# Optimization experiments

Hardware: AMD Instinct MI355X
Metric: run time of the kernel (lower is better)

The kernel has to match this reference:

```python
import jax, jax.numpy as jnp
import numpy as np

HID = 128
N_LAYERS = 6


def _init_linear(key, fan_in, fan_out, scale=None):
    kw, kb = jax.random.split(key)
    s = scale if scale is not None else (1.0 / np.sqrt(fan_in))
    W = jax.random.uniform(kw, (fan_in, fan_out), jnp.float32, -s, s)
    b = jnp.zeros((fan_out,), jnp.float32)
    return W, b


def setup_inputs() -> dict:
    key = jax.random.key(0)
    ks = jax.random.split(key, 16)
    N, E, EC = 50000, 600000, 100000
    x = jax.random.normal(ks[0], (N, 9), jnp.float32)
    edge_index = jax.random.randint(ks[1], (2, E), 0, N, jnp.int64)
    edge_attr = jax.random.normal(ks[2], (E, 11), jnp.float32)
    connectivity = jax.random.randint(ks[3], (EC, 2), 0, N, jnp.int64)
    bc_disp = (jax.random.uniform(ks[4], (N, 1)) < 0.1).astype(jnp.float32)
    prop_I22 = jax.random.uniform(ks[5], (EC,), jnp.float32)

    enc_W1, enc_b1 = _init_linear(ks[6], 9, HID)
    enc_W2, enc_b2 = _init_linear(ks[7], HID, HID)
    # per-layer GN params stacked along axis 0
    msg_in = 2 * HID + 11
    mk = jax.random.split(ks[8], N_LAYERS)
    uk = jax.random.split(ks[9], N_LAYERS)
    mk2 = jax.random.split(ks[10], N_LAYERS)
    msg_W1 = jnp.stack([_init_linear(mk[i], msg_in, HID)[0] for i in range(N_LAYERS)])
    msg_b1 = jnp.zeros((N_LAYERS, HID), jnp.float32)
    msg_W2 = jnp.stack([_init_linear(mk2[i], HID, HID)[0] for i in range(N_LAYERS)])
    msg_b2 = jnp.zeros((N_LAYERS, HID), jnp.float32)
    upd_W = jnp.stack([_init_linear(uk[i], 2 * HID, HID)[0] for i in range(N_LAYERS)])
    upd_b = jnp.zeros((N_LAYERS, HID), jnp.float32)

    ef_W1, ef_b1 = _init_linear(ks[11], 1 + 2 * HID, 64)
    ef_W2, ef_b2 = _init_linear(ks[12], 64, 64)
    ef_W3, ef_b3 = _init_linear(ks[13], 64, 3, scale=0.1 * np.sqrt(6.0 / (64 + 3)))

    return dict(x=x, edge_index=edge_index, edge_attr=edge_attr,
                connectivity=connectivity, bc_disp=bc_disp, prop_I22=prop_I22,
                n_quad_pts=5,
                enc_W1=enc_W1, enc_b1=enc_b1, enc_W2=enc_W2, enc_b2=enc_b2,
                msg_W1=msg_W1, msg_b1=msg_b1, msg_W2=msg_W2, msg_b2=msg_b2,
                upd_W=upd_W, upd_b=upd_b,
                ef_W1=ef_W1, ef_b1=ef_b1, ef_W2=ef_W2, ef_b2=ef_b2,
                ef_W3=ef_W3, ef_b3=ef_b3)


def reference(x, edge_index, edge_attr, connectivity, bc_disp, prop_I22, n_quad_pts,
              enc_W1, enc_b1, enc_W2, enc_b2,
              msg_W1, msg_b1, msg_W2, msg_b2, upd_W, upd_b,
              ef_W1, ef_b1, ef_W2, ef_b2, ef_W3, ef_b3):
    N = x.shape[0]
    silu = jax.nn.silu
    # encoder MLP
    h = silu(x @ enc_W1 + enc_b1)
    h = silu(h @ enc_W2 + enc_b2)
    src, dst = edge_index[0], edge_index[1]
    for l in range(N_LAYERS):
        m_in = jnp.concatenate([h[src], h[dst], edge_attr], axis=-1)  # (E, 2H+11)
        m = silu(m_in @ msg_W1[l] + msg_b1[l]) @ msg_W2[l] + msg_b2[l]
        agg = jax.ops.segment_sum(m, dst, num_segments=N)  # scatter-add
        h = jnp.concatenate([h, agg], axis=-1) @ upd_W[l] + upd_b[l] + h  # residual update
        h = silu(h)
    # continuous edge field evaluation
    n1, n2 = connectivity[:, 0], connectivity[:, 1]
    EC = connectivity.shape[0]
    xi_1d = jnp.linspace(0.0, 1.0, n_quad_pts, dtype=jnp.float32)
    xi = jnp.broadcast_to(xi_1d[None, :, None], (EC, n_quad_pts, 1))
    h_i = jnp.broadcast_to(h[n1][:, None, :], (EC, n_quad_pts, HID))
    h_j = jnp.broadcast_to(h[n2][:, None, :], (EC, n_quad_pts, HID))
    inp = jnp.concatenate([xi, h_i, h_j], axis=-1)  # (EC, n_pts, 1+2H)
    f = silu(inp @ ef_W1 + ef_b1)
    f = silu(f @ ef_W2 + ef_b2)
    fields = f @ ef_W3 + ef_b3  # (EC, n_pts, 3)
    # hard BCs
    bc_mask = bc_disp[:, 0]
    bc_i, bc_j = bc_mask[n1], bc_mask[n2]
    xi_vals = xi[..., 0]
    mask_i = 1.0 - bc_i[:, None] * (1.0 - xi_vals)
    mask_j = 1.0 - bc_j[:, None] * xi_vals
    fields = fields * (mask_i * mask_j)[..., None]
    return h, xi, fields, prop_I22
```

## Files before the change

kernel.cpp:

```cpp
#include <hip/hip_runtime.h>
#include <hip/hip_bf16.h>

#define HID 128
#define EA_DIM 11
#define MSG_IN (2 * HID + EA_DIM)
#define TILE_E 128
#define KCAP 272
#define KB (KCAP * 2)
#define MSG_LDS 139264

typedef __attribute__((ext_vector_type(8))) short short8;
typedef __attribute__((ext_vector_type(16))) float f32x16;
typedef __attribute__((ext_vector_type(4))) float float4v;

__device__ __forceinline__ float siluf(float x) { return x / (1.f + __expf(-x)); }
__device__ __forceinline__ short f2bf(float f) {
    __hip_bfloat16 h = __float2bfloat16(f);
    return *reinterpret_cast<short*>(&h);
}
__device__ __forceinline__ int crow(int r, int khalf) { return (r & 3) + 8 * (r >> 2) + 4 * khalf; }

__global__ __launch_bounds__(128) void encoder_kernel(
    const float* __restrict__ x, const float* __restrict__ W1, const float* __restrict__ b1,
    const float* __restrict__ W2, const float* __restrict__ b2,
    float* __restrict__ h, short* __restrict__ hb)
{
    int i = blockIdx.x, j = threadIdx.x;
    __shared__ float xs[9];
    __shared__ float t1[HID];
    if (j < 9) xs[j] = x[(size_t)i * 9 + j];
    __syncthreads();
    float acc = b1[j];
    #pragma unroll
    for (int k = 0; k < 9; ++k) acc = fmaf(xs[k], W1[k * HID + j], acc);
    t1[j] = siluf(acc);
    __syncthreads();
    float acc2 = b2[j];
    #pragma unroll 8
    for (int k = 0; k < HID; ++k) acc2 = fmaf(t1[k], W2[k * HID + j], acc2);
    float v = siluf(acc2);
    h[(size_t)i * HID + j] = v;
    if (hb) hb[(size_t)i * HID + j] = f2bf(v);
}

__global__ void convert_w_kernel(
    const float* __restrict__ msgW1, const float* __restrict__ msgW2,
    const float* __restrict__ updW,
    const float* __restrict__ efW1, const float* __restrict__ efW2, const float* __restrict__ efW3,
    short* __restrict__ w1t, short* __restrict__ w2t, short* __restrict__ updwt,
    short* __restrict__ efw1t, short* __restrict__ efw2t, short* __restrict__ efw3t, int nl)
{
    int gid = blockIdx.x * blockDim.x + threadIdx.x;
    int n1 = nl * 128 * (KCAP / 8);
    int n2 = nl * 128 * (HID / 8);
    int n3 = nl * 128 * 32;
    int n4 = 64 * 32, n5 = 64 * 8, n6 = 32 * 8;
    short8 v;
    if (gid < n1) {
        int c = gid % (KCAP / 8);
        int rem = gid / (KCAP / 8);
        int n = rem % 128, lay = rem / 128;
        #pragma unroll
        for (int j = 0; j < 8; ++j) {
            int k = c * 8 + j;
            v[j] = (k < MSG_IN) ? f2bf(msgW1[(size_t)lay * MSG_IN * HID + (size_t)k * HID + n]) : (short)0;
        }
        *(short8*)(w1t + ((size_t)lay * 128 + n) * KCAP + c * 8) = v;
    } else if (gid < n1 + n2) {
        int g = gid - n1;
        int c = g % (HID / 8);
        int rem = g / (HID / 8);
        int n = rem % 128, lay = rem / 128;
        #pragma unroll
        for (int j = 0; j < 8; ++j)
            v[j] = f2bf(msgW2[(size_t)lay * HID * HID + (size_t)(c * 8 + j) * HID + n]);
        *(short8*)(w2t + ((size_t)lay * 128 + n) * HID + c * 8) = v;
    } else if (gid < n1 + n2 + n3) {
        int g = gid - n1 - n2;
        int c = g & 31;
        int rem = g >> 5;
        int n = rem & 127, lay = rem >> 7;
        #pragma unroll
        for (int j = 0; j < 8; ++j)
            v[j] = f2bf(updW[(size_t)lay * 256 * 128 + (size_t)(c * 8 + j) * 128 + n]);
        *(short8*)(updwt + ((size_t)lay * 128 + n) * 256 + c * 8) = v;
    } else if (gid < n1 + n2 + n3 + n4) {
        int g = gid - n1 - n2 - n3;
        int c = g & 31, n = g >> 5;
        #pragma unroll
        for (int j = 0; j < 8; ++j)
            v[j] = f2bf(efW1[(size_t)(c * 8 + j + 1) * 64 + n]);
        *(short8*)(efw1t + (size_t)n * 256 + c * 8) = v;
    } else if (gid < n1 + n2 + n3 + n4 + n5) {
        int g = gid - n1 - n2 - n3 - n4;
        int c = g & 7, n = g >> 3;
        #pragma unroll
        for (int j = 0; j < 8; ++j)
            v[j] = f2bf(efW2[(size_t)(c * 8 + j) * 64 + n]);
        *(short8*)(efw2t + (size_t)n * 64 + c * 8) = v;
    } else if (gid < n1 + n2 + n3 + n4 + n5 + n6) {
        int g = gid - n1 - n2 - n3 - n4 - n5;
        int c = g & 7, n = g >> 3;
        #pragma unroll
        for (int j = 0; j < 8; ++j)
            v[j] = (n < 3) ? f2bf(efW3[(size_t)(c * 8 + j) * 3 + n]) : (short)0;
        *(short8*)(efw3t + (size_t)n * 64 + c * 8) = v;
    }
}

__global__ void hist_kernel(const int* __restrict__ ei, int* __restrict__ cnt, int E)
{
    for (int e = blockIdx.x * blockDim.x + threadIdx.x; e < E; e += gridDim.x * blockDim.x)
        atomicAdd(&cnt[ei[(size_t)E + e]], 1);
}
__global__ __launch_bounds__(256) void scanA_kernel(const int* __restrict__ cnt, int* __restrict__ btot, int N)
{
    __shared__ int s[256];
    int i = blockIdx.x * 256 + threadIdx.x;
    s[threadIdx.x] = (i < N) ? cnt[i] : 0;
    __syncthreads();
    for (int o = 128; o > 0; o >>= 1) {
        if (threadIdx.x < o) s[threadIdx.x] += s[threadIdx.x + o];
        __syncthreads();
    }
    if (threadIdx.x == 0) btot[blockIdx.x] = s[0];
}
__global__ __launch_bounds__(1024) void scanB_kernel(int* __restrict__ btot, int nb)
{
    __shared__ int s[1024];
    int t = threadIdx.x;
    int v = (t < nb) ? btot[t] : 0;
    s[t] = v;
    __syncthreads();
    for (int o = 1; o < 1024; o <<= 1) {
        int tv = 0;
        if (t >= o) tv = s[t - o];
        __syncthreads();
        s[t] += tv;
        __syncthreads();
    }
    if (t < nb) btot[t] = s[t] - v;
}
__global__ __launch_bounds__(256) void scanC_kernel(const int* __restrict__ cnt, const int* __restrict__ btot,
                                                    int* __restrict__ cur, int N)
{
    __shared__ int s[256];
    int i = blockIdx.x * 256 + threadIdx.x;
    int t = threadIdx.x;
    int v = (i < N) ? cnt[i] : 0;
    s[t] = v;
    __syncthreads();
    for (int o = 1; o < 256; o <<= 1) {
        int tv = 0;
        if (t >= o) tv = s[t - o];
        __syncthreads();
        s[t] += tv;
        __syncthreads();
    }
    if (i < N) cur[i] = btot[blockIdx.x] + s[t] - v;
}
__global__ void scatter_kernel(const int* __restrict__ ei, int* __restrict__ cur,
                               int* __restrict__ eord, int E)
{
    for (int e = blockIdx.x * blockDim.x + threadIdx.x; e < E; e += gridDim.x * blockDim.x) {
        int d = ei[(size_t)E + e];
        int p = atomicAdd(&cur[d], 1);
        eord[p] = e;
    }
}
__global__ void reorder_kernel(const int* __restrict__ ei, const float* __restrict__ ea,
                               const int* __restrict__ eord,
                               int* __restrict__ srcs_s, int* __restrict__ dsts_s,
                               short* __restrict__ ea_s, int E)
{
    for (int p = blockIdx.x * blockDim.x + threadIdx.x; p < E; p += gridDim.x * blockDim.x) {
        int es = eord[p];
        srcs_s[p] = ei[es];
        dsts_s[p] = ei[(size_t)E + es];
        short tv[16];
        #pragma unroll
        for (int j = 0; j < 16; ++j) tv[j] = 0;
        #pragma unroll
        for (int j = 0; j < EA_DIM; ++j) tv[j] = f2bf(ea[(size_t)es * EA_DIM + j]);
        short8 v0, v1;
        #pragma unroll
        for (int j = 0; j < 8; ++j) { v0[j] = tv[j]; v1[j] = tv[8 + j]; }
        *(short8*)(ea_s + (size_t)p * 16) = v0;
        *(short8*)(ea_s + (size_t)p * 16 + 8) = v1;
    }
}

__global__ __launch_bounds__(512, 1) void msg_mfma_kernel(
    const float* __restrict__ h, const short* __restrict__ hb,
    const int* __restrict__ ei, const float* __restrict__ ea,
    const int* __restrict__ srcs_s, const int* __restrict__ dsts_s, const short* __restrict__ ea_s,
    const short* __restrict__ w1t, const float* __restrict__ b1,
    const short* __restrict__ w2t, const float* __restrict__ b2,
    float* __restrict__ agg, int E, int ntiles)
{
    extern __shared__ char smem[];
    char* sA = smem + 69632;
    __shared__ int dsts[TILE_E];

    int tid = threadIdx.x, ln = tid & 63, wave = tid >> 6;
    int mh = wave & 1, nq4 = wave >> 1;
    int l31 = ln & 31, khalf = ln >> 5;

    {
        int row = tid & 127, grp = tid >> 7;
        for (int c = grp; c < 34; c += 4) {
            short8 v = *(const short8*)(w1t + (size_t)row * KCAP + c * 8);
            *(short8*)(smem + ((row * KB + c * 16) ^ ((row & 7) << 4))) = v;
        }
    }

    int col = nq4 * 32 + l31;
    float b1v = b1[col], b2v = b2[col];
    short8 zer;
    #pragma unroll
    for (int j = 0; j < 8; ++j) zer[j] = 0;
    int ar0 = mh * 64 + l31;
    const short8* w2r = (const short8*)(w2t + (size_t)col * HID);

    #pragma unroll 1
    for (int tile = blockIdx.x; tile < ntiles; tile += gridDim.x) {
        __syncthreads();

        {
            int r = tid >> 2, q = tid & 3;
            long ep = (long)tile * TILE_E + r;
            bool valid = ep < E;
            int idx = 0;
            if (valid) {
                if (ea_s) idx = (q < 2) ? srcs_s[ep] : dsts_s[ep];
                else      idx = (q < 2) ? ei[ep] : ei[(size_t)E + ep];
            }
            int half = q & 1;
            int dbase = (q >> 1) * 256 + half * 128;
            if (hb) {
                const short8* hr8 = (const short8*)(hb + (size_t)idx * HID + half * 64);
                #pragma unroll
                for (int c = 0; c < 8; ++c) {
                    short8 v = valid ? hr8[c] : zer;
                    *(short8*)(sA + ((r * KB + dbase + c * 16) ^ ((r & 7) << 4))) = v;
                }
            } else {
                const float* hr = h + (size_t)idx * HID + half * 64;
                #pragma unroll
                for (int c = 0; c < 8; ++c) {
                    short8 v = zer;
                    if (valid) {
                        float4v f0 = *(const float4v*)(hr + c * 8);
                        float4v f1 = *(const float4v*)(hr + c * 8 + 4);
                        #pragma unroll
                        for (int j = 0; j < 4; ++j) { v[j] = f2bf(f0[j]); v[4 + j] = f2bf(f1[j]); }
                    }
                    *(short8*)(sA + ((r * KB + dbase + c * 16) ^ ((r & 7) << 4))) = v;
                }
            }
            if (q == 2) dsts[r] = valid ? idx : -1;
            if (q == 3) {
                short8 v0 = zer, v1 = zer;
                if (valid) {
                    if (ea_s) {
                        v0 = *(const short8*)(ea_s + (size_t)ep * 16);
                        v1 = *(const short8*)(ea_s + (size_t)ep * 16 + 8);
                    } else {
                        short tv[16];
                        #pragma unroll
                        for (int j = 0; j < 16; ++j) tv[j] = 0;
                        #pragma unroll
                        for (int j = 0; j < EA_DIM; ++j) tv[j] = f2bf(ea[(size_t)ep * EA_DIM + j]);
                        #pragma unroll
                        for (int j = 0; j < 8; ++j) { v0[j] = tv[j]; v1[j] = tv[8 + j]; }
                    }
                }
                *(short8*)(sA + ((r * KB + 512) ^ ((r & 7) << 4))) = v0;
                *(short8*)(sA + ((r * KB + 528) ^ ((r & 7) << 4))) = v1;
            }
        }
        __syncthreads();

        f32x16 acc1[2] = {};
        for (int kk = 0; kk < 17; ++kk) {
            int kb = kk * 32 + khalf * 16;
            short8 a0 = *(short8*)(sA + ((ar0 * KB + kb) ^ ((ar0 & 7) << 4)));
            short8 a1 = *(short8*)(sA + (((ar0 + 32) * KB + kb) ^ (((ar0 + 32) & 7) << 4)));
            short8 w  = *(short8*)(smem + ((col * KB + kb) ^ ((col & 7) << 4)));
            acc1[0] = __builtin_amdgcn_mfma_f32_32x32x16_bf16(a0, w, acc1[0], 0, 0, 0);
            acc1[1] = __builtin_amdgcn_mfma_f32_32x32x16_bf16(a1, w, acc1[1], 0, 0, 0);
        }
        __syncthreads();

        #pragma unroll
        for (int mi = 0; mi < 2; ++mi)
            #pragma unroll
            for (int r = 0; r < 16; ++r) {
                float s = siluf(acc1[mi][r] + b1v);
                int row = mh * 64 + mi * 32 + crow(r, khalf);
                *(short*)(sA + ((row * 256 + col * 2) ^ ((row & 7) << 4))) = f2bf(s);
            }
        __syncthreads();

        f32x16 acc2[2];
        #pragma unroll
        for (int mi = 0; mi < 2; ++mi)
            #pragma unroll
            for (int r = 0; r < 16; ++r) acc2[mi][r] = b2v;
        for (int kk = 0; kk < 8; ++kk) {
            int kb = kk * 32 + khalf * 16;
            short8 a0 = *(short8*)(sA + ((ar0 * 256 + kb) ^ ((ar0 & 7) << 4)));
            short8 a1 = *(short8*)(sA + (((ar0 + 32) * 256 + kb) ^ (((ar0 + 32) & 7) << 4)));
            short8 w  = w2r[kk * 2 + khalf];
            acc2[0] = __builtin_amdgcn_mfma_f32_32x32x16_bf16(a0, w, acc2[0], 0, 0, 0);
            acc2[1] = __builtin_amdgcn_mfma_f32_32x32x16_bf16(a1, w, acc2[1], 0, 0, 0);
        }

        if (ea_s) {
            __syncthreads();
            #pragma unroll
            for (int mi = 0; mi < 2; ++mi)
                #pragma unroll
                for (int r = 0; r < 16; ++r) {
                    int row = mh * 64 + mi * 32 + crow(r, khalf);
                    *(float*)(sA + row * 512 + col * 4) = acc2[mi][r];
                }
            __syncthreads();
            {
                int c2 = tid & 63, g = tid >> 6;
                float s0 = 0.f, s1 = 0.f;
                int dprev = -1;
                #pragma unroll 1
                for (int rr = 0; rr < 16; ++rr) {
                    int row = g * 16 + rr;
                    int d = dsts[row];
                    float2 v = *(float2*)(sA + row * 512 + c2 * 8);
                    if (d != dprev) {
                        if (dprev >= 0) {
                            atomicAdd(agg + (size_t)dprev * HID + c2 * 2,     s0);
                            atomicAdd(agg + (size_t)dprev * HID + c2 * 2 + 1, s1);
                        }
                        s0 = 0.f; s1 = 0.f; dprev = d;
                    }
                    if (d >= 0) { s0 += v.x; s1 += v.y; }
                }
                if (dprev >= 0) {
                    atomicAdd(agg + (size_t)dprev * HID + c2 * 2,     s0);
                    atomicAdd(agg + (size_t)dprev * HID + c2 * 2 + 1, s1);
                }
            }
        } else {
            #pragma unroll
            for (int mi = 0; mi < 2; ++mi)
                #pragma unroll
                for (int r = 0; r < 16; ++r) {
                    int row = mh * 64 + mi * 32 + crow(r, khalf);
                    int d = dsts[row];
                    if (d >= 0) atomicAdd(agg + (size_t)d * HID + col, acc2[mi][r]);
                }
        }
    }
}

__global__ __launch_bounds__(256) void upd_mfma_kernel(
    float* __restrict__ h, short* __restrict__ hb, const float* __restrict__ agg,
    const short* __restrict__ updwt, const float* __restrict__ b, int N, int ntiles)
{
    __shared__ char sA[64 * 512];
    int tid = threadIdx.x, ln = tid & 63, wave = tid >> 6;
    int mhalf = wave & 1, nhalf = wave >> 1, l31 = ln & 31, khalf = ln >> 5;
    float bv[2];
    #pragma unroll
    for (int ni = 0; ni < 2; ++ni) bv[ni] = b[nhalf * 64 + ni * 32 + l31];
    short8 zer;
    #pragma unroll
    for (int j = 0; j < 8; ++j) zer[j] = 0;

    #pragma unroll 1
    for (int tile = blockIdx.x; tile < ntiles; tile += gridDim.x) {
        __syncthreads();
        {
            int r = tid >> 2, q = tid & 3;
            int node = tile * 64 + r;
            bool valid = node < N;
            if (q < 2) {
                if (hb) {
                    const short8* hr8 = (const short8*)(hb + (size_t)node * HID + (q & 1) * 64);
                    #pragma unroll
                    for (int c = 0; c < 8; ++c) {
                        short8 v = valid ? hr8[c] : zer;
                        *(short8*)(sA + ((r * 512 + (q & 1) * 128 + c * 16) ^ ((r & 7) << 4))) = v;
                    }
                } else {
                    const float* hr = h + (size_t)node * HID + (q & 1) * 64;
                    #pragma unroll
                    for (int c = 0; c < 8; ++c) {
                        short8 v = zer;
                        if (valid) {
                            float4v f0 = *(const float4v*)(hr + c * 8);
                            float4v f1 = *(const float4v*)(hr + c * 8 + 4);
                            #pragma unroll
                            for (int j = 0; j < 4; ++j) { v[j] = f2bf(f0[j]); v[4 + j] = f2bf(f1[j]); }
                        }
                        *(short8*)(sA + ((r * 512 + (q & 1) * 128 + c * 16) ^ ((r & 7) << 4))) = v;
                    }
                }
            } else {
                const float* ar = agg + (size_t)node * HID + (q & 1) * 64;
                #pragma unroll
                for (int c = 0; c < 8; ++c) {
                    short8 v = zer;
                    if (valid) {
                        float4v f0 = *(const float4v*)(ar + c * 8);
                        float4v f1 = *(const float4v*)(ar + c * 8 + 4);
                        #pragma unroll
                        for (int j = 0; j < 4; ++j) { v[j] = f2bf(f0[j]); v[4 + j] = f2bf(f1[j]); }
                    }
                    *(short8*)(sA + ((r * 512 + 256 + (q & 1) * 128 + c * 16) ^ ((r & 7) << 4))) = v;
                }
            }
        }
        __syncthreads();
        f32x16 acc[2] = {};
        int arow = mhalf * 32 + l31;
        const short* bp0 = updwt + (size_t)(nhalf * 64 + l31) * 256 + khalf * 8;
        const short* bp1 = updwt + (size_t)(nhalf * 64 + 32 + l31) * 256 + khalf * 8;
        for (int kk = 0; kk < 16; ++kk) {
            short8 a  = *(short8*)(sA + ((arow * 512 + kk * 32 + khalf * 16) ^ ((arow & 7) << 4)));
            short8 w0 = *(const short8*)(bp0 + kk * 16);
            short8 w1 = *(const short8*)(bp1 + kk * 16);
            acc[0] = __builtin_amdgcn_mfma_f32_32x32x16_bf16(a, w0, acc[0], 0, 0, 0);
            acc[1] = __builtin_amdgcn_mfma_f32_32x32x16_bf16(a, w1, acc[1], 0, 0, 0);
        }
        #pragma unroll
        for (int ni = 0; ni < 2; ++ni) {
            int col = nhalf * 64 + ni * 32 + l31;
            #pragma unroll
            for (int r = 0; r < 16; ++r) {
                int node = tile * 64 + mhalf * 32 + crow(r, khalf);
                if (node < N) {
                    float val = siluf(acc[ni][r] + bv[ni] + h[(size_t)node * HID + col]);
                    h[(size_t)node * HID + col] = val;
                    if (hb) hb[(size_t)node * HID + col] = f2bf(val);
                }
            }
        }
    }
}

__global__ __launch_bounds__(256) void fields_mfma_kernel(
    const float* __restrict__ h, const short* __restrict__ hb,
    const int* __restrict__ conn, const float* __restrict__ bc,
    const float* __restrict__ efW1, const float* __restrict__ efb1,
    const float* __restrict__ efb2, const float* __restrict__ efb3,
    const short* __restrict__ efw1t, const short* __restrict__ efw2t, const short* __restrict__ efw3t,
    float* __restrict__ f_out, int EC, int nq, int ntiles)
{
    __shared__ char sA1[64 * 512];
    __shared__ char sA2[64 * 128];
    __shared__ char sF2[64 * 128];
    __shared__ float bcis[64], bcjs[64];
    int tid = threadIdx.x, ln = tid & 63, wave = tid >> 6;
    int mhalf = wave & 1, nhalf = wave >> 1, l31 = ln & 31, khalf = ln >> 5;
    int col = nhalf * 32 + l31;
    float w1x = efW1[col];
    float b1v = efb1[col], b2v = efb2[col];
    float b3v = (l31 < 3) ? efb3[l31] : 0.f;
    float inv = (nq > 1) ? 1.f / (float)(nq - 1) : 0.f;
    short8 zer;
    #pragma unroll
    for (int j = 0; j < 8; ++j) zer[j] = 0;

    #pragma unroll 1
    for (int tile = blockIdx.x; tile < ntiles; tile += gridDim.x) {
        __syncthreads();
        {
            int r = tid >> 2, q = tid & 3;
            long p = (long)tile * 64 + r;
            bool valid = p < EC;
            int node = 0;
            if (valid) node = conn[p * 2 + (q >> 1)];
            if (q == 0) {
                bcis[r] = valid ? bc[conn[p * 2]] : 0.f;
                bcjs[r] = valid ? bc[conn[p * 2 + 1]] : 0.f;
            }
            int cbyte = (q >> 1) * 256 + (q & 1) * 128;
            if (hb) {
                const short8* hr8 = (const short8*)(hb + (size_t)node * HID + (q & 1) * 64);
                #pragma unroll
                for (int c = 0; c < 8; ++c) {
                    short8 v = valid ? hr8[c] : zer;
                    *(short8*)(sA1 + ((r * 512 + cbyte + c * 16) ^ ((r & 7) << 4))) = v;
                }
            } else {
                const float* hr = h + (size_t)node * HID + (q & 1) * 64;
                #pragma unroll
                for (int c = 0; c < 8; ++c) {
                    short8 v = zer;
                    if (valid) {
                        float4v f0 = *(const float4v*)(hr + c * 8);
                        float4v f1 = *(const float4v*)(hr + c * 8 + 4);
                        #pragma unroll
                        for (int j = 0; j < 4; ++j) { v[j] = f2bf(f0[j]); v[4 + j] = f2bf(f1[j]); }
                    }
                    *(short8*)(sA1 + ((r * 512 + cbyte + c * 16) ^ ((r & 7) << 4))) = v;
                }
            }
        }
        __syncthreads();
        f32x16 hp = {};
        int arow = mhalf * 32 + l31;
        for (int kk = 0; kk < 16; ++kk) {
            short8 a = *(short8*)(sA1 + ((arow * 512 + kk * 32 + khalf * 16) ^ ((arow & 7) << 4)));
            short8 b = *(const short8*)(efw1t + (size_t)col * 256 + kk * 16 + khalf * 8);
            hp = __builtin_amdgcn_mfma_f32_32x32x16_bf16(a, b, hp, 0, 0, 0);
        }
        #pragma unroll
        for (int r = 0; r < 16; ++r) hp[r] += b1v;

        for (int q = 0; q < nq; ++q) {
            float xi = (float)q * inv;
            #pragma unroll
            for (int r = 0; r < 16; ++r) {
                float f1 = siluf(fmaf(xi, w1x, hp[r]));
                int row = mhalf * 32 + crow(r, khalf);
                *(short*)(sA2 + ((row * 128 + col * 2) ^ ((row & 7) << 4))) = f2bf(f1);
            }
            __syncthreads();
            f32x16 f2a = {};
            for (int kk = 0; kk < 4; ++kk) {
                short8 a = *(short8*)(sA2 + ((arow * 128 + kk * 32 + khalf * 16) ^ ((l31 & 7) << 4)));
                short8 b = *(const short8*)(efw2t + (size_t)col * 64 + kk * 16 + khalf * 8);
                f2a = __builtin_amdgcn_mfma_f32_32x32x16_bf16(a, b, f2a, 0, 0, 0);
            }
            #pragma unroll
            for (int r = 0; r < 16; ++r) {
                float f2 = siluf(f2a[r] + b2v);
                int row = mhalf * 32 + crow(r, khalf);
                *(short*)(sF2 + ((row * 128 + col * 2) ^ ((row & 7) << 4))) = f2bf(f2);
            }
            __syncthreads();
            f32x16 oa = {};
            for (int kk = 0; kk < 4; ++kk) {
                short8 a = *(short8*)(sF2 + ((arow * 128 + kk * 32 + khalf * 16) ^ ((l31 & 7) << 4)));
                short8 b = *(const short8*)(efw3t + (size_t)l31 * 64 + kk * 16 + khalf * 8);
                oa = __builtin_amdgcn_mfma_f32_32x32x16_bf16(a, b, oa, 0, 0, 0);
            }
            if (nhalf == 0 && l31 < 3) {
                #pragma unroll
                for (int r = 0; r < 16; ++r) {
                    int row = mhalf * 32 + crow(r, khalf);
                    long p = (long)tile * 64 + row;
                    if (p < EC) {
                        float mask = (1.f - bcis[row] * (1.f - xi)) * (1.f - bcjs[row] * xi);
                        f_out[((size_t)p * nq + q) * 3 + l31] = (oa[r] + b3v) * mask;
                    }
                }
            }
        }
    }
}

__global__ void aux_kernel(const float* __restrict__ prop, float* __restrict__ out_p,
                           float* __restrict__ out_xi, int EC, int nq, float inv)
{
    int i = blockIdx.x * blockDim.x + threadIdx.x;
    if (i < EC) out_p[i] = prop[i];
    if (i < EC * nq) out_xi[i] = (float)(i % nq) * inv;
}

extern "C" void kernel_launch(void* const* d_in, const int* in_sizes, int n_in,
                              void* d_out, int out_size, void* d_ws, size_t ws_size,
                              hipStream_t stream) {
    const float* x     = (const float*)d_in[0];
    const int*   ei    = (const int*)d_in[1];
    const float* ea    = (const float*)d_in[2];
    const int*   conn  = (const int*)d_in[3];
    const float* bc    = (const float*)d_in[4];
    const float* prop  = (const float*)d_in[5];
    const float* encW1 = (const float*)d_in[7];
    const float* encb1 = (const float*)d_in[8];
    const float* encW2 = (const float*)d_in[9];
    const float* encb2 = (const float*)d_in[10];
    const float* msgW1 = (const float*)d_in[11];
    const float* msgb1 = (const float*)d_in[12];
    const float* msgW2 = (const float*)d_in[13];
    const float* msgb2 = (const float*)d_in[14];
    const float* updW  = (const float*)d_in[15];
    const float* updb  = (const float*)d_in[16];
    const float* efW1  = (const float*)d_in[17];
    const float* efb1  = (const float*)d_in[18];
    const float* efW2  = (const float*)d_in[19];
    const float* efb2  = (const float*)d_in[20];
    const float* efW3  = (const float*)d_in[21];
    const float* efb3  = (const float*)d_in[22];

    int N  = in_sizes[0] / 9;
    int E  = in_sizes[1] / 2;
    int EC = in_sizes[5];
    int nl = in_sizes[11] / (MSG_IN * HID);
    int nq = (int)(((long long)out_size - (long long)N * HID - EC) / (4LL * EC));

    float* out    = (float*)d_out;
    float* h      = out;
    float* out_xi = out + (size_t)N * HID;
    float* out_f  = out_xi + (size_t)EC * nq;
    float* out_p  = out_f + (size_t)EC * nq * 3;

    size_t w1t_e = (size_t)nl * 128 * KCAP;
    size_t w2t_e = (size_t)nl * 128 * HID;
    size_t updwt_e = (size_t)nl * 128 * 256;
    size_t efw1t_e = 64 * 256, efw2t_e = 64 * 64, efw3t_e = 32 * 64;
    short* w1t   = (short*)d_ws;
    short* w2t   = w1t + w1t_e;
    short* updwt = w2t + w2t_e;
    short* efw1t = updwt + updwt_e;
    short* efw2t = efw1t + efw1t_e;
    short* efw3t = efw2t + efw2t_e;
    size_t wbytes = (w1t_e + w2t_e + updwt_e + efw1t_e + efw2t_e + efw3t_e) * 2;
    wbytes = (wbytes + 255) & ~(size_t)255;
    size_t hb_bytes  = (size_t)N * HID * 2;
    size_t agg_bytes = (size_t)N * HID * 4;
    size_t sort_bytes = ((size_t)2 * N + 1024 + (size_t)3 * E) * 4 + (size_t)E * 32;

    short* hb = nullptr;
    float* agg;
    int *icnt = nullptr, *icur = nullptr, *btot = nullptr, *eord = nullptr;
    int *srcs_s = nullptr, *dsts_s = nullptr;
    short* ea_s = nullptr;
    if (ws_size >= wbytes + hb_bytes + agg_bytes + sort_bytes) {
        char* p = (char*)d_ws + wbytes;
        hb = (short*)p;      p += hb_bytes;
        agg = (float*)p;     p += agg_bytes;
        icnt = (int*)p;      p += (size_t)N * 4;
        icur = (int*)p;      p += (size_t)N * 4;
        btot = (int*)p;      p += 1024 * 4;
        eord = (int*)p;      p += (size_t)E * 4;
        srcs_s = (int*)p;    p += (size_t)E * 4;
        dsts_s = (int*)p;    p += (size_t)E * 4;
        ea_s = (short*)p;
    } else if (ws_size >= wbytes + hb_bytes + agg_bytes) {
        hb  = (short*)((char*)d_ws + wbytes);
        agg = (float*)((char*)d_ws + wbytes + hb_bytes);
    } else {
        agg = (float*)((char*)d_ws + wbytes);
    }

    hipFuncSetAttribute((const void*)msg_mfma_kernel,
                        hipFuncAttributeMaxDynamicSharedMemorySize, MSG_LDS);

    encoder_kernel<<<N, 128, 0, stream>>>(x, encW1, encb1, encW2, encb2, h, hb);

    {
        int chunks = nl * 128 * (KCAP / 8) + nl * 128 * (HID / 8) + nl * 128 * 32
                   + 64 * 32 + 64 * 8 + 32 * 8;
        convert_w_kernel<<<(chunks + 255) / 256, 256, 0, stream>>>(
            msgW1, msgW2, updW, efW1, efW2, efW3,
            w1t, w2t, updwt, efw1t, efw2t, efw3t, nl);
    }

    if (ea_s) {
        int nb = (N + 255) / 256;
        hipMemsetAsync(icnt, 0, (size_t)N * 4, stream);
        hist_kernel<<<512, 256, 0, stream>>>(ei, icnt, E);
        scanA_kernel<<<nb, 256, 0, stream>>>(icnt, btot, N);
        scanB_kernel<<<1, 1024, 0, stream>>>(btot, nb);
        scanC_kernel<<<nb, 256, 0, stream>>>(icnt, btot, icur, N);
        scatter_kernel<<<512, 256, 0, stream>>>(ei, icur, eord, E);
        reorder_kernel<<<512, 256, 0, stream>>>(ei, ea, eord, srcs_s, dsts_s, ea_s, E);
    }

    int ntiles = (E + TILE_E - 1) / TILE_E;
    int utiles = (N + 63) / 64;
    for (int l = 0; l < nl; ++l) {
        hipMemsetAsync(agg, 0, agg_bytes, stream);
        msg_mfma_kernel<<<256, 512, MSG_LDS, stream>>>(
            h, hb, ei, ea, srcs_s, dsts_s, ea_s,
            w1t + (size_t)l * 128 * KCAP, msgb1 + (size_t)l * HID,
            w2t + (size_t)l * 128 * HID,  msgb2 + (size_t)l * HID,
            agg, E, ntiles);
        upd_mfma_kernel<<<512, 256, 0, stream>>>(
            h, hb, agg, updwt + (size_t)l * 128 * 256, updb + (size_t)l * HID, N, utiles);
    }

    int ftiles = (EC + 63) / 64;
    fields_mfma_kernel<<<512, 256, 0, stream>>>(
        h, hb, conn, bc, efW1, efb1, efb2, efb3, efw1t, efw2t, efw3t,
        out_f, EC, nq, ftiles);

    float inv = (nq > 1) ? 1.f / (float)(nq - 1) : 0.f;
    aux_kernel<<<(EC * nq + 255) / 256, 256, 0, stream>>>(prop, out_p, out_xi, EC, nq, inv);
}
```

Measured before the change: 1.929 ms.

## Prefetch next tile's gathered node rows into registers during MFMA compute

In the sorted-edge path, the message kernel now loads the next tile's source and destination hidden rows and edge attributes into registers right after the current tile is staged to LDS. The loads are in flight while the two MFMA GEMMs run, hiding gather latency behind compute. The cost is about 40 extra VGPRs per thread for the prefetch buffers, which may lower occupancy or cause spills. The old branch that handled sorted data inside the generic load path is removed.

```diff
diff --git a/kernel.cpp b/kernel.cpp
--- a/kernel.cpp
+++ b/kernel.cpp
@@ -222,19 +222,48 @@
     int ar0 = mh * 64 + l31;
     const short8* w2r = (const short8*)(w2t + (size_t)col * HID);
 
+    bool sorted = (ea_s != nullptr) && (hb != nullptr);
+
+    int pr = tid >> 2, pq = tid & 3;
+    int pf_idx = 0; bool pf_valid = false;
+    short8 pf_h[8];
+    short8 pf_e0 = zer, pf_e1 = zer;
+
+    if (sorted) {
+        long ep = (long)blockIdx.x * TILE_E + pr;
+        pf_valid = ep < E;
+        pf_idx = pf_valid ? ((pq < 2) ? srcs_s[ep] : dsts_s[ep]) : 0;
+        const short8* hr8 = (const short8*)(hb + (size_t)pf_idx * HID + (pq & 1) * 64);
+        #pragma unroll
+        for (int c = 0; c < 8; ++c) pf_h[c] = hr8[c];
+        if (pq == 3 && pf_valid) {
+            pf_e0 = *(const short8*)(ea_s + (size_t)ep * 16);
+            pf_e1 = *(const short8*)(ea_s + (size_t)ep * 16 + 8);
+        }
+    }
+
     #pragma unroll 1
     for (int tile = blockIdx.x; tile < ntiles; tile += gridDim.x) {
         __syncthreads();
 
-        {
-            int r = tid >> 2, q = tid & 3;
+        if (sorted) {
+            int dbase = (pq >> 1) * 256 + (pq & 1) * 128;
+            #pragma unroll
+            for (int c = 0; c < 8; ++c) {
+                short8 v = pf_valid ? pf_h[c] : zer;
+                *(short8*)(sA + ((pr * KB + dbase + c * 16) ^ ((pr & 7) << 4))) = v;
+            }
+            if (pq == 2) dsts[pr] = pf_valid ? pf_idx : -1;
+            if (pq == 3) {
+                *(short8*)(sA + ((pr * KB + 512) ^ ((pr & 7) << 4))) = pf_valid ? pf_e0 : zer;
+                *(short8*)(sA + ((pr * KB + 528) ^ ((pr & 7) << 4))) = pf_valid ? pf_e1 : zer;
+            }
+        } else {
+            int r = pr, q = pq;
             long ep = (long)tile * TILE_E + r;
             bool valid = ep < E;
             int idx = 0;
-            if (valid) {
-                if (ea_s) idx = (q < 2) ? srcs_s[ep] : dsts_s[ep];
-                else      idx = (q < 2) ? ei[ep] : ei[(size_t)E + ep];
-            }
+            if (valid) idx = (q < 2) ? ei[ep] : ei[(size_t)E + ep];
             int half = q & 1;
             int dbase = (q >> 1) * 256 + half * 128;
             if (hb) {
@@ -262,24 +291,32 @@
             if (q == 3) {
                 short8 v0 = zer, v1 = zer;
                 if (valid) {
-                    if (ea_s) {
-                        v0 = *(const short8*)(ea_s + (size_t)ep * 16);
-                        v1 = *(const short8*)(ea_s + (size_t)ep * 16 + 8);
-                    } else {
-                        short tv[16];
-                        #pragma unroll
-                        for (int j = 0; j < 16; ++j) tv[j] = 0;
-                        #pragma unroll
-                        for (int j = 0; j < EA_DIM; ++j) tv[j] = f2bf(ea[(size_t)ep * EA_DIM + j]);
-                        #pragma unroll
-                        for (int j = 0; j < 8; ++j) { v0[j] = tv[j]; v1[j] = tv[8 + j]; }
-                    }
+                    short tv[16];
+                    #pragma unroll
+                    for (int j = 0; j < 16; ++j) tv[j] = 0;
+                    #pragma unroll
+                    for (int j = 0; j < EA_DIM; ++j) tv[j] = f2bf(ea[(size_t)ep * EA_DIM + j]);
+                    #pragma unroll
+                    for (int j = 0; j < 8; ++j) { v0[j] = tv[j]; v1[j] = tv[8 + j]; }
                 }
                 *(short8*)(sA + ((r * KB + 512) ^ ((r & 7) << 4))) = v0;
                 *(short8*)(sA + ((r * KB + 528) ^ ((r & 7) << 4))) = v1;
             }
         }
         __syncthreads();
+
+        if (sorted) {
+            long ep = (long)(tile + gridDim.x) * TILE_E + pr;
+            pf_valid = ep < E;
+            pf_idx = pf_valid ? ((pq < 2) ? srcs_s[ep] : dsts_s[ep]) : 0;
+            const short8* hr8 = (const short8*)(hb + (size_t)pf_idx * HID + (pq & 1) * 64);
+            #pragma unroll
+            for (int c = 0; c < 8; ++c) pf_h[c] = hr8[c];
+            if (pq == 3 && pf_valid) {
+                pf_e0 = *(const short8*)(ea_s + (size_t)ep * 16);
+                pf_e1 = *(const short8*)(ea_s + (size_t)ep * 16 + 8);
+            }
+        }
 
         f32x16 acc1[2] = {};
         for (int kk = 0; kk < 17; ++kk) {
@@ -316,7 +353,7 @@
             acc2[1] = __builtin_amdgcn_mfma_f32_32x32x16_bf16(a1, w, acc2[1], 0, 0, 0);
         }
 
-        if (ea_s) {
+        if (sorted) {
             __syncthreads();
             #pragma unroll
             for (int mi = 0; mi < 2; ++mi)
```

Measured after the change: 1.760 ms. 1.1x faster.
